# Kernel tuning notes

Hardware: AMD Instinct MI355X
Metric: run time of the kernel (lower is better)

The kernel has to match this reference:

```python
import jax, jax.numpy as jnp
import numpy as np
import math

B, S, H, NH = 1, 2048, 1024, 16  # batch, seq, hidden, heads


def setup_inputs() -> dict:
    key = jax.random.key(0)
    ks = jax.random.split(key, 12)
    inp = {
        "query": jax.random.normal(ks[0], (B, S, H), dtype=jnp.float32),
        "key": jax.random.normal(ks[1], (B, S, H), dtype=jnp.float32),
        "value": jax.random.normal(ks[2], (B, S, H), dtype=jnp.float32),
        "attention_mask": jax.random.randint(ks[3], (1, 1, S, S), 0, 2, dtype=jnp.int32),
        # torch nn.Linear params: y = x @ W.T + b, W init ~ U(-1/sqrt(H), 1/sqrt(H))
        "Wq": jax.random.uniform(ks[4], (H, H), jnp.float32, -1, 1) / math.sqrt(H),
        "bq": jax.random.uniform(ks[5], (H,), jnp.float32, -1, 1) / math.sqrt(H),
        "Wk": jax.random.uniform(ks[6], (H, H), jnp.float32, -1, 1) / math.sqrt(H),
        "bk": jax.random.uniform(ks[7], (H,), jnp.float32, -1, 1) / math.sqrt(H),
        "Wv": jax.random.uniform(ks[8], (H, H), jnp.float32, -1, 1) / math.sqrt(H),
        "bv": jax.random.uniform(ks[9], (H,), jnp.float32, -1, 1) / math.sqrt(H),
        "Wo": jax.random.uniform(ks[10], (H, H), jnp.float32, -1, 1) / math.sqrt(H),
        "bo": jax.random.uniform(ks[11], (H,), jnp.float32, -1, 1) / math.sqrt(H),
        "head": NH,
        "hidden_size": H,
    }
    return inp


def reference(query, key, value, attention_mask, Wq, bq, Wk, bk, Wv, bv, Wo, bo, head, hidden_size):
    b, s, _ = query.shape
    d_k = hidden_size // head

    def proj(x, W, bias):
        # [b, s, hidden] -> [b, head, s, d_k]
        y = x @ W.T + bias
        return y.reshape(b, s, head, d_k).transpose(0, 2, 1, 3)

    q = proj(query, Wq, bq)
    k = proj(key, Wk, bk)
    v = proj(value, Wv, bv)

    # naive full score matrix, as in the source (scale by sqrt(d_k) = last dim of q)
    scores = jnp.einsum("bhqd,bhkd->bhqk", q, k) / math.sqrt(d_k)
    # faithful quirk: masked positions are set to 0 (not -inf) before softmax
    scores = jnp.where(attention_mask == 0, jnp.zeros((), scores.dtype), scores)
    attn = jax.nn.softmax(scores, axis=-1)

    out = jnp.einsum("bhqk,bhkd->bhqd", attn, v)  # [b, head, s, d_k]
    out = out.transpose(0, 2, 1, 3).reshape(b, s, head * d_k)
    return out @ Wo.T + bo
```

## Files before the change

### kernel.cpp

```cpp
#include <hip/hip_runtime.h>
#include <hip/hip_bf16.h>


#define S_LEN 2048
#define HID   1024
#define NHEAD 16
#define DK    64

typedef unsigned short u16;
typedef __attribute__((ext_vector_type(8))) short bf16x8;
typedef __attribute__((ext_vector_type(4))) short bf16x4;
typedef __attribute__((ext_vector_type(4))) float f32x4;

__device__ __forceinline__ void load16_lds(const void* g, void* l) {
  __builtin_amdgcn_global_load_lds(
      (const __attribute__((address_space(1))) void*)g,
      (__attribute__((address_space(3))) void*)l, 16, 0, 0);
}

__device__ __forceinline__ short bfbits(float x) {
  __hip_bfloat16 h = __float2bfloat16(x);
  return *(short*)&h;
}
__device__ __forceinline__ bf16x8 cvt8(float4 a, float4 b) {
  bf16x8 r;
  r[0] = bfbits(a.x); r[1] = bfbits(a.y); r[2] = bfbits(a.z); r[3] = bfbits(a.w);
  r[4] = bfbits(b.x); r[5] = bfbits(b.y); r[6] = bfbits(b.z); r[7] = bfbits(b.w);
  return r;
}
__device__ __forceinline__ float bf2f(u16 u) {
  unsigned v = (unsigned)u << 16;
  return *(float*)&v;
}

__global__ __launch_bounds__(256) void cvtW_kernel(
    const float* __restrict__ wq, const float* __restrict__ wk,
    const float* __restrict__ wv, const float* __restrict__ wo,
    u16* __restrict__ Wbf) {
  const int y = blockIdx.y;
  const float* src = y == 0 ? wq : (y == 1 ? wk : (y == 2 ? wv : wo));
  size_t i = ((size_t)blockIdx.x * 256 + threadIdx.x) * 8;
  float4 a = *(const float4*)(src + i);
  float4 b = *(const float4*)(src + i + 4);
  *(bf16x8*)(Wbf + (size_t)y * (HID * HID) + i) = cvt8(a, b);
}

__global__ void pack_mask_kernel(const int* __restrict__ mask,
                                 unsigned int* __restrict__ bits) {
  int w = blockIdx.x * blockDim.x + threadIdx.x;
  const int4* p = (const int4*)(mask + (size_t)w * 32);
  unsigned word = 0;
#pragma unroll
  for (int i = 0; i < 8; ++i) {
    int4 v = p[i];
    word |= (unsigned)(v.x != 0) << (i * 4 + 0);
    word |= (unsigned)(v.y != 0) << (i * 4 + 1);
    word |= (unsigned)(v.z != 0) << (i * 4 + 2);
    word |= (unsigned)(v.w != 0) << (i * 4 + 3);
  }
  bits[w] = word;
}

template <int BM, bool ABF>
__global__ __launch_bounds__(512) void gemm_bt(
    const void* A0, const void* A1, const void* A2,
    const u16* __restrict__ Wbase,
    const float* b0, const float* b1, const float* b2,
    void* C0, void* C1, void* C2,
    int store_fp32, int transpose_z2, int qscale_z0) {
  constexpr int Mm = 2048, Nn = 1024, Kk = 1024, BK = 64;
  constexpr int NIT = Kk / BK;
  constexpr int MT = BM / 32;
  constexpr int MTILES = Mm / BM;
  constexpr int AG = BM / 16;
  constexpr int AU = BM / 64;

  const int z = blockIdx.z;
  const void* A    = z == 0 ? A0 : (z == 1 ? A1 : A2);
  const u16*  W    = Wbase + (size_t)z * (Nn * Kk);
  const float* bias = z == 0 ? b0 : (z == 1 ? b1 : b2);
  void*       C    = z == 0 ? C0 : (z == 1 ? C1 : C2);
  const int transpose = (z == 2) ? transpose_z2 : 0;
  const float oscale = (z == 0 && qscale_z0) ? 0.125f : 1.0f;

  const int tid = threadIdx.x, lane = tid & 63, wave = tid >> 6;
  const int q4 = lane >> 4, c16 = lane & 15;
  const int bLin = blockIdx.x + blockIdx.y * gridDim.x;
  const int mBase = (bLin % MTILES) * BM;
  const int nBase = (bLin / MTILES) * 128;
  const int wm = (wave >> 2) * (BM / 2), wn = (wave & 3) * 32;

  __shared__ __align__(16) u16 As[2][2][BM * 32];
  __shared__ __align__(16) u16 Bs[2][2][128 * 32];

  f32x4 acc[MT][2] = {};

  const int srow = lane >> 2;
  const int se8  = (lane & 3) * 8;

  const u16*   Ab = (const u16*)A;
  const float* Af = (const float*)A;

  auto issueW = [&](int it, int buf) {
#pragma unroll
    for (int j = 0; j < 2; ++j) {
      int u = wave * 2 + j;
      int h = u >> 3, grp = u & 7;
      load16_lds(W + (size_t)(nBase + grp * 16 + srow) * Kk + it * BK +
                     h * 32 + se8,
                 &Bs[buf][h][grp * 512]);
    }
  };
  auto issueA = [&](int it, int buf) {
#pragma unroll
    for (int j = 0; j < AU; ++j) {
      int u = wave * AU + j;
      int h = u / AG, grp = u % AG;
      load16_lds(Ab + (size_t)(mBase + grp * 16 + srow) * Kk + it * BK +
                     h * 32 + se8,
                 &As[buf][h][grp * 512]);
    }
  };
  float4 ar[AU][2];
  auto loadA = [&](int it) {
#pragma unroll
    for (int j = 0; j < AU; ++j) {
      int u = wave * AU + j;
      int h = u / AG, grp = u % AG;
      const float* s = Af + (size_t)(mBase + grp * 16 + srow) * Kk + it * BK +
                       h * 32 + se8;
      ar[j][0] = *(const float4*)s;
      ar[j][1] = *(const float4*)(s + 4);
    }
  };
  auto storeA = [&](int buf) {
#pragma unroll
    for (int j = 0; j < AU; ++j) {
      int u = wave * AU + j;
      int h = u / AG, grp = u % AG;
      *(bf16x8*)&As[buf][h][grp * 512 + srow * 32 + se8] =
          cvt8(ar[j][0], ar[j][1]);
    }
  };

  issueW(0, 0);
  if (ABF) issueA(0, 0);
  else { loadA(0); storeA(0); }
  __syncthreads();

  for (int it = 0; it < NIT; ++it) {
    const int buf = it & 1, nbuf = buf ^ 1;
    if (it + 1 < NIT) {
      issueW(it + 1, nbuf);
      if (ABF) issueA(it + 1, nbuf);
      else     loadA(it + 1);
    }
#pragma unroll
    for (int kk = 0; kk < 2; ++kk) {
      bf16x8 af[MT], bfr[2];
#pragma unroll
      for (int t = 0; t < MT; ++t)
        af[t] = *(const bf16x8*)&As[buf][kk][(wm + t * 16 + c16) * 32 + q4 * 8];
#pragma unroll
      for (int t = 0; t < 2; ++t)
        bfr[t] = *(const bf16x8*)&Bs[buf][kk][(wn + t * 16 + c16) * 32 + q4 * 8];
#pragma unroll
      for (int mt = 0; mt < MT; ++mt)
#pragma unroll
        for (int nt = 0; nt < 2; ++nt)
          acc[mt][nt] = __builtin_amdgcn_mfma_f32_16x16x32_bf16(
              af[mt], bfr[nt], acc[mt][nt], 0, 0, 0);
    }
    if (!ABF && it + 1 < NIT) storeA(nbuf);
    __syncthreads();
  }

#pragma unroll
  for (int nt = 0; nt < 2; ++nt) {
    int col = nBase + wn + nt * 16 + c16;
    float bv = bias[col];
#pragma unroll
    for (int mt = 0; mt < MT; ++mt) {
#pragma unroll
      for (int r = 0; r < 4; ++r) {
        int row = mBase + wm + mt * 16 + q4 * 4 + r;
        float v = (acc[mt][nt][r] + bv) * oscale;
        if (store_fp32)
          ((float*)C)[(size_t)row * Nn + col] = v;
        else if (transpose)
          ((__hip_bfloat16*)C)[(size_t)col * Mm + row] = __float2bfloat16(v);
        else
          ((__hip_bfloat16*)C)[(size_t)row * Nn + col] = __float2bfloat16(v);
      }
    }
  }
}

__global__ __launch_bounds__(512) void attn_kernel(
    const u16* __restrict__ Qb, const u16* __restrict__ Kb,
    const u16* __restrict__ Vt, const unsigned* __restrict__ mbits,
    u16* __restrict__ partO, float* __restrict__ partL) {
  constexpr int NITA = S_LEN / 2 / 64;
  const int qt = blockIdx.x, h = blockIdx.y, zz = blockIdx.z;
  const int tid = threadIdx.x, lane = tid & 63, wave = tid >> 6;
  const int q4 = lane >> 4, c16 = lane & 15;

  __shared__ __align__(16) u16 Ks[2][2][64 * 32];
  __shared__ __align__(16) u16 Vs[2][2][64 * 32];
  __shared__ __align__(16) u16 Ps[8][16 * 72];

  const int wq0 = qt * 128 + wave * 16;

  bf16x8 qf[2];
#pragma unroll
  for (int kk = 0; kk < 2; ++kk)
    qf[kk] = *(const bf16x8*)(Qb + (size_t)(wq0 + c16) * HID + h * DK +
                              kk * 32 + q4 * 8);

  f32x4 o[4] = {};
  float l_lane[4] = {};

  const int srow = lane >> 2;
  const int se8  = (lane & 3) * 8;
  const int kvbase = zz * (S_LEN / 2);

  auto issueKV = [&](int it, int buf) {
    const int kv0 = kvbase + it * 64;
#pragma unroll
    for (int j = 0; j < 2; ++j) {
      int i = wave * 2 + j;
      if (i < 8) {
        int half = i >> 2, grp = i & 3;
        load16_lds(Kb + (size_t)(kv0 + grp * 16 + srow) * HID + h * DK +
                       half * 32 + se8,
                   &Ks[buf][half][grp * 512]);
      } else {
        int ii = i - 8;
        int half = ii >> 2, grp = ii & 3;
        load16_lds(Vt + (size_t)(h * DK + grp * 16 + srow) * S_LEN + kv0 +
                       half * 32 + se8,
                   &Vs[buf][half][grp * 512]);
      }
    }
  };

  issueKV(0, 0);
  __syncthreads();

  for (int it = 0; it < NITA; ++it) {
    const int buf = it & 1, nbuf = buf ^ 1;
    const int kv0 = kvbase + it * 64;
    if (it + 1 < NITA) issueKV(it + 1, nbuf);

    f32x4 sv[4];
#pragma unroll
    for (int nt = 0; nt < 4; ++nt) {
      bf16x8 kf0 = *(const bf16x8*)&Ks[buf][0][(nt * 16 + c16) * 32 + q4 * 8];
      bf16x8 kf1 = *(const bf16x8*)&Ks[buf][1][(nt * 16 + c16) * 32 + q4 * 8];
      f32x4 a = {};
      a = __builtin_amdgcn_mfma_f32_16x16x32_bf16(qf[0], kf0, a, 0, 0, 0);
      a = __builtin_amdgcn_mfma_f32_16x16x32_bf16(qf[1], kf1, a, 0, 0, 0);
      sv[nt] = a;
    }

#pragma unroll
    for (int r = 0; r < 4; ++r) {
      int row = wq0 + q4 * 4 + r;
      const unsigned* mrow = mbits + (size_t)row * 64 + (kv0 >> 5);
      unsigned w0 = mrow[0], w1 = mrow[1];
#pragma unroll
      for (int nt = 0; nt < 4; ++nt) {
        unsigned word = (nt < 2) ? w0 : w1;
        int bit = ((nt & 1) * 16) + c16;
        float s = ((word >> bit) & 1u) ? sv[nt][r] : 0.0f;
        float p = __expf(s);
        sv[nt][r] = p;
        l_lane[r] += p;
      }
    }

    u16* pw = &Ps[wave][0];
#pragma unroll
    for (int r = 0; r < 4; ++r)
#pragma unroll
      for (int nt = 0; nt < 4; ++nt)
        ((__hip_bfloat16*)pw)[(q4 * 4 + r) * 72 + nt * 16 + c16] =
            __float2bfloat16(sv[nt][r]);
    asm volatile("s_waitcnt lgkmcnt(0)" ::: "memory");

#pragma unroll
    for (int kk = 0; kk < 2; ++kk) {
      bf16x8 pa = *(const bf16x8*)&pw[c16 * 72 + kk * 32 + q4 * 8];
#pragma unroll
      for (int nt = 0; nt < 4; ++nt) {
        bf16x8 vb = *(const bf16x8*)&Vs[buf][kk][(nt * 16 + c16) * 32 + q4 * 8];
        o[nt] = __builtin_amdgcn_mfma_f32_16x16x32_bf16(pa, vb, o[nt], 0, 0, 0);
      }
    }
    __syncthreads();
  }

#pragma unroll
  for (int r = 0; r < 4; ++r) {
    float s = l_lane[r];
#pragma unroll
    for (int d = 1; d < 16; d <<= 1) s += __shfl_xor(s, d);
    l_lane[r] = s;
  }

#pragma unroll
  for (int r = 0; r < 4; ++r) {
    int row = wq0 + q4 * 4 + r;
#pragma unroll
    for (int nt = 0; nt < 4; ++nt)
      ((__hip_bfloat16*)partO)[((size_t)zz * S_LEN + row) * HID + h * DK +
                               nt * 16 + c16] = __float2bfloat16(o[nt][r]);
    if (c16 == 0)
      partL[((size_t)zz * NHEAD + h) * S_LEN + row] = l_lane[r];
  }
}

__global__ __launch_bounds__(256) void combine_kernel(
    const u16* __restrict__ partO, const float* __restrict__ partL,
    u16* __restrict__ ctx) {
  size_t idx = ((size_t)blockIdx.x * 256 + threadIdx.x) * 4;
  int row = (int)(idx >> 10);
  int col = (int)(idx & 1023);
  int h = col >> 6;
  float l = partL[(size_t)h * S_LEN + row] +
            partL[((size_t)NHEAD + h) * S_LEN + row];
  float inv = 1.0f / l;
  bf16x4 a = *(const bf16x4*)(partO + idx);
  bf16x4 b = *(const bf16x4*)(partO + (size_t)S_LEN * HID + idx);
  bf16x4 r;
#pragma unroll
  for (int j = 0; j < 4; ++j) {
    float v = (bf2f((u16)a[j]) + bf2f((u16)b[j])) * inv;
    r[j] = bfbits(v);
  }
  *(bf16x4*)(ctx + idx) = r;
}

extern "C" void kernel_launch(void* const* d_in, const int* in_sizes, int n_in,
                              void* d_out, int out_size, void* d_ws, size_t ws_size,
                              hipStream_t stream) {
  const float* q    = (const float*)d_in[0];
  const float* k    = (const float*)d_in[1];
  const float* v    = (const float*)d_in[2];
  const int*   mask = (const int*)d_in[3];
  const float* Wq = (const float*)d_in[4];
  const float* bq = (const float*)d_in[5];
  const float* Wk = (const float*)d_in[6];
  const float* bk = (const float*)d_in[7];
  const float* Wv = (const float*)d_in[8];
  const float* bv = (const float*)d_in[9];
  const float* Wo = (const float*)d_in[10];
  const float* bo = (const float*)d_in[11];

  const size_t M2 = (size_t)S_LEN * HID;
  const size_t need = (4 + 2 + 2 + 2 + 2) * M2 * 2 +
                      (size_t)S_LEN * 64 * 4 + 2 * NHEAD * S_LEN * 4;
  if (ws_size < need) return;

  u16* Wbf   = (u16*)d_ws;
  u16* partO = Wbf + 4 * (size_t)HID * HID / 2 * 2;
  u16* Qb    = partO + 2 * M2;
  u16* Kb    = Qb + M2;
  u16* Vt    = Kb + M2;
  unsigned* mbits = (unsigned*)(Vt + M2);
  float* partL = (float*)(mbits + (size_t)S_LEN * 64);
  u16* ctx = Qb;

  hipLaunchKernelGGL(cvtW_kernel, dim3(512, 4), dim3(256), 0, stream,
                     Wq, Wk, Wv, Wo, Wbf);

  hipLaunchKernelGGL(pack_mask_kernel, dim3((S_LEN * (S_LEN / 32)) / 256),
                     dim3(256), 0, stream, mask, mbits);

  hipLaunchKernelGGL((gemm_bt<128, false>), dim3(8, 16, 3), dim3(512), 0,
                     stream, q, k, v, Wbf, bq, bk, bv,
                     (void*)Qb, (void*)Kb, (void*)Vt, 0, 1, 1);

  hipLaunchKernelGGL(attn_kernel, dim3(S_LEN / 128, NHEAD, 2), dim3(512), 0,
                     stream, Qb, Kb, Vt, mbits, partO, partL);

  hipLaunchKernelGGL(combine_kernel, dim3((S_LEN * HID / 4) / 256), dim3(256),
                     0, stream, partO, partL, ctx);

  hipLaunchKernelGGL((gemm_bt<64, true>), dim3(8, 32, 1), dim3(512), 0,
                     stream, ctx, ctx, ctx, Wbf + 3 * (size_t)HID * HID,
                     bo, bo, bo, d_out, d_out, d_out, 1, 0, 0);
}
```

Before: 213.5 us.

## Pre-convert QKV inputs to bf16 and retile projection GEMMs with smaller blocks

Adds a pre-pass that converts the fp32 query/key/value activations to bf16 together with the weights, so the QKV GEMM can stream both operands into LDS with direct global-to-LDS loads instead of register-staged fp32 conversion. The QKV and output GEMMs become dedicated kernels with 256-thread blocks and smaller M tiles (64 and 32 rows), giving more blocks for better CU occupancy. The cost is an extra full read and write pass over the activations and less operand reuse per block.

```diff
diff --git a/kernel.cpp b/kernel.cpp
--- a/kernel.cpp
+++ b/kernel.cpp
@@ -33,16 +33,31 @@
   return *(float*)&v;
 }
 
-__global__ __launch_bounds__(256) void cvtW_kernel(
-    const float* __restrict__ wq, const float* __restrict__ wk,
-    const float* __restrict__ wv, const float* __restrict__ wo,
+__global__ __launch_bounds__(256) void cvt_kernel(
+    const float* __restrict__ q, const float* __restrict__ k,
+    const float* __restrict__ v, const float* __restrict__ wq,
+    const float* __restrict__ wk, const float* __restrict__ wv,
+    const float* __restrict__ wo, u16* __restrict__ Xbf,
     u16* __restrict__ Wbf) {
   const int y = blockIdx.y;
-  const float* src = y == 0 ? wq : (y == 1 ? wk : (y == 2 ? wv : wo));
   size_t i = ((size_t)blockIdx.x * 256 + threadIdx.x) * 8;
+  const float* src;
+  u16* dst;
+  size_t n;
+  if (y < 3) {
+    src = y == 0 ? q : (y == 1 ? k : v);
+    dst = Xbf + (size_t)y * (S_LEN * HID);
+    n = (size_t)S_LEN * HID;
+  } else {
+    int w = y - 3;
+    src = w == 0 ? wq : (w == 1 ? wk : (w == 2 ? wv : wo));
+    dst = Wbf + (size_t)w * (HID * HID);
+    n = (size_t)HID * HID;
+  }
+  if (i >= n) return;
   float4 a = *(const float4*)(src + i);
   float4 b = *(const float4*)(src + i + 4);
-  *(bf16x8*)(Wbf + (size_t)y * (HID * HID) + i) = cvt8(a, b);
+  *(bf16x8*)(dst + i) = cvt8(a, b);
 }
 
 __global__ void pack_mask_kernel(const int* __restrict__ mask,
@@ -61,133 +76,86 @@
   bits[w] = word;
 }
 
-template <int BM, bool ABF>
-__global__ __launch_bounds__(512) void gemm_bt(
-    const void* A0, const void* A1, const void* A2,
-    const u16* __restrict__ Wbase,
-    const float* b0, const float* b1, const float* b2,
-    void* C0, void* C1, void* C2,
-    int store_fp32, int transpose_z2, int qscale_z0) {
-  constexpr int Mm = 2048, Nn = 1024, Kk = 1024, BK = 64;
-  constexpr int NIT = Kk / BK;
-  constexpr int MT = BM / 32;
-  constexpr int MTILES = Mm / BM;
-  constexpr int AG = BM / 16;
-  constexpr int AU = BM / 64;
-
+__global__ __launch_bounds__(256) void gemm_qkv(
+    const u16* __restrict__ Xbf, const u16* __restrict__ Wbf,
+    const float* __restrict__ bq, const float* __restrict__ bk,
+    const float* __restrict__ bv, u16* __restrict__ Qb,
+    u16* __restrict__ Kb, u16* __restrict__ Vt) {
+  constexpr int Mm = 2048, Nn = 1024, Kk = 1024, NIT = 16;
   const int z = blockIdx.z;
-  const void* A    = z == 0 ? A0 : (z == 1 ? A1 : A2);
-  const u16*  W    = Wbase + (size_t)z * (Nn * Kk);
-  const float* bias = z == 0 ? b0 : (z == 1 ? b1 : b2);
-  void*       C    = z == 0 ? C0 : (z == 1 ? C1 : C2);
-  const int transpose = (z == 2) ? transpose_z2 : 0;
-  const float oscale = (z == 0 && qscale_z0) ? 0.125f : 1.0f;
+  const u16* A = Xbf + (size_t)z * (S_LEN * HID);
+  const u16* W = Wbf + (size_t)z * (HID * HID);
+  const float* bias = z == 0 ? bq : (z == 1 ? bk : bv);
+  u16* C = z == 0 ? Qb : (z == 1 ? Kb : Vt);
+  const float oscale = (z == 0) ? 0.125f : 1.0f;
+  const int transpose = (z == 2);
 
   const int tid = threadIdx.x, lane = tid & 63, wave = tid >> 6;
   const int q4 = lane >> 4, c16 = lane & 15;
-  const int bLin = blockIdx.x + blockIdx.y * gridDim.x;
-  const int mBase = (bLin % MTILES) * BM;
-  const int nBase = (bLin / MTILES) * 128;
-  const int wm = (wave >> 2) * (BM / 2), wn = (wave & 3) * 32;
-
-  __shared__ __align__(16) u16 As[2][2][BM * 32];
+  const int bx = blockIdx.x;
+  const int mBase = (bx & 31) * 64;
+  const int nBase = (bx >> 5) * 128;
+  const int wn = wave * 32;
+
+  __shared__ __align__(16) u16 As[2][2][64 * 32];
   __shared__ __align__(16) u16 Bs[2][2][128 * 32];
 
-  f32x4 acc[MT][2] = {};
-
-  const int srow = lane >> 2;
-  const int se8  = (lane & 3) * 8;
-
-  const u16*   Ab = (const u16*)A;
-  const float* Af = (const float*)A;
-
-  auto issueW = [&](int it, int buf) {
+  f32x4 acc[4][2] = {};
+  const int srow = lane >> 2, se8 = (lane & 3) * 8;
+
+  auto issue = [&](int it, int buf) {
 #pragma unroll
     for (int j = 0; j < 2; ++j) {
-      int u = wave * 2 + j;
-      int h = u >> 3, grp = u & 7;
-      load16_lds(W + (size_t)(nBase + grp * 16 + srow) * Kk + it * BK +
+      int u = wave * 2 + j, h = u >> 2, grp = u & 3;
+      load16_lds(A + (size_t)(mBase + grp * 16 + srow) * Kk + it * 64 +
+                     h * 32 + se8,
+                 &As[buf][h][grp * 512]);
+    }
+#pragma unroll
+    for (int j = 0; j < 4; ++j) {
+      int u = wave * 4 + j, h = u >> 3, grp = u & 7;
+      load16_lds(W + (size_t)(nBase + grp * 16 + srow) * Kk + it * 64 +
                      h * 32 + se8,
                  &Bs[buf][h][grp * 512]);
     }
   };
-  auto issueA = [&](int it, int buf) {
-#pragma unroll
-    for (int j = 0; j < AU; ++j) {
-      int u = wave * AU + j;
-      int h = u / AG, grp = u % AG;
-      load16_lds(Ab + (size_t)(mBase + grp * 16 + srow) * Kk + it * BK +
-                     h * 32 + se8,
-                 &As[buf][h][grp * 512]);
-    }
-  };
-  float4 ar[AU][2];
-  auto loadA = [&](int it) {
-#pragma unroll
-    for (int j = 0; j < AU; ++j) {
-      int u = wave * AU + j;
-      int h = u / AG, grp = u % AG;
-      const float* s = Af + (size_t)(mBase + grp * 16 + srow) * Kk + it * BK +
-                       h * 32 + se8;
-      ar[j][0] = *(const float4*)s;
-      ar[j][1] = *(const float4*)(s + 4);
-    }
-  };
-  auto storeA = [&](int buf) {
-#pragma unroll
-    for (int j = 0; j < AU; ++j) {
-      int u = wave * AU + j;
-      int h = u / AG, grp = u % AG;
-      *(bf16x8*)&As[buf][h][grp * 512 + srow * 32 + se8] =
-          cvt8(ar[j][0], ar[j][1]);
-    }
-  };
-
-  issueW(0, 0);
-  if (ABF) issueA(0, 0);
-  else { loadA(0); storeA(0); }
+
+  issue(0, 0);
   __syncthreads();
 
   for (int it = 0; it < NIT; ++it) {
     const int buf = it & 1, nbuf = buf ^ 1;
-    if (it + 1 < NIT) {
-      issueW(it + 1, nbuf);
-      if (ABF) issueA(it + 1, nbuf);
-      else     loadA(it + 1);
-    }
+    if (it + 1 < NIT) issue(it + 1, nbuf);
 #pragma unroll
     for (int kk = 0; kk < 2; ++kk) {
-      bf16x8 af[MT], bfr[2];
-#pragma unroll
-      for (int t = 0; t < MT; ++t)
-        af[t] = *(const bf16x8*)&As[buf][kk][(wm + t * 16 + c16) * 32 + q4 * 8];
+      bf16x8 af[4], bfr[2];
+#pragma unroll
+      for (int t = 0; t < 4; ++t)
+        af[t] = *(const bf16x8*)&As[buf][kk][(t * 16 + c16) * 32 + q4 * 8];
 #pragma unroll
       for (int t = 0; t < 2; ++t)
         bfr[t] = *(const bf16x8*)&Bs[buf][kk][(wn + t * 16 + c16) * 32 + q4 * 8];
 #pragma unroll
-      for (int mt = 0; mt < MT; ++mt)
+      for (int mt = 0; mt < 4; ++mt)
 #pragma unroll
         for (int nt = 0; nt < 2; ++nt)
           acc[mt][nt] = __builtin_amdgcn_mfma_f32_16x16x32_bf16(
               af[mt], bfr[nt], acc[mt][nt], 0, 0, 0);
     }
-    if (!ABF && it + 1 < NIT) storeA(nbuf);
     __syncthreads();
   }
 
 #pragma unroll
   for (int nt = 0; nt < 2; ++nt) {
     int col = nBase + wn + nt * 16 + c16;
-    float bv = bias[col];
-#pragma unroll
-    for (int mt = 0; mt < MT; ++mt) {
+    float bv2 = bias[col];
+#pragma unroll
+    for (int mt = 0; mt < 4; ++mt) {
 #pragma unroll
       for (int r = 0; r < 4; ++r) {
-        int row = mBase + wm + mt * 16 + q4 * 4 + r;
-        float v = (acc[mt][nt][r] + bv) * oscale;
-        if (store_fp32)
-          ((float*)C)[(size_t)row * Nn + col] = v;
-        else if (transpose)
+        int row = mBase + mt * 16 + q4 * 4 + r;
+        float v = (acc[mt][nt][r] + bv2) * oscale;
+        if (transpose)
           ((__hip_bfloat16*)C)[(size_t)col * Mm + row] = __float2bfloat16(v);
         else
           ((__hip_bfloat16*)C)[(size_t)row * Nn + col] = __float2bfloat16(v);
@@ -339,6 +307,78 @@
     r[j] = bfbits(v);
   }
   *(bf16x4*)(ctx + idx) = r;
+}
+
+__global__ __launch_bounds__(256) void gemm_out(
+    const u16* __restrict__ ctx, const u16* __restrict__ Wo,
+    const float* __restrict__ bo, float* __restrict__ out) {
+  constexpr int Nn = 1024, Kk = 1024, NIT = 16;
+  const int tid = threadIdx.x, lane = tid & 63, wave = tid >> 6;
+  const int q4 = lane >> 4, c16 = lane & 15;
+  const int bx = blockIdx.x;
+  const int mBase = (bx & 63) * 32;
+  const int nBase = (bx >> 6) * 128;
+  const int wn = wave * 32;
+
+  __shared__ __align__(16) u16 As[2][2][32 * 32];
+  __shared__ __align__(16) u16 Bs[2][2][128 * 32];
+
+  f32x4 acc[2][2] = {};
+  const int srow = lane >> 2, se8 = (lane & 3) * 8;
+
+  auto issue = [&](int it, int buf) {
+    {
+      int u = wave, h = u >> 1, grp = u & 1;
+      load16_lds(ctx + (size_t)(mBase + grp * 16 + srow) * Kk + it * 64 +
+                     h * 32 + se8,
+                 &As[buf][h][grp * 512]);
+    }
+#pragma unroll
+    for (int j = 0; j < 4; ++j) {
+      int u = wave * 4 + j, h = u >> 3, grp = u & 7;
+      load16_lds(Wo + (size_t)(nBase + grp * 16 + srow) * Kk + it * 64 +
+                     h * 32 + se8,
+                 &Bs[buf][h][grp * 512]);
+    }
+  };
+
+  issue(0, 0);
+  __syncthreads();
+
+  for (int it = 0; it < NIT; ++it) {
+    const int buf = it & 1, nbuf = buf ^ 1;
+    if (it + 1 < NIT) issue(it + 1, nbuf);
+#pragma unroll
+    for (int kk = 0; kk < 2; ++kk) {
+      bf16x8 af[2], bfr[2];
+#pragma unroll
+      for (int t = 0; t < 2; ++t)
+        af[t] = *(const bf16x8*)&As[buf][kk][(t * 16 + c16) * 32 + q4 * 8];
+#pragma unroll
+      for (int t = 0; t < 2; ++t)
+        bfr[t] = *(const bf16x8*)&Bs[buf][kk][(wn + t * 16 + c16) * 32 + q4 * 8];
+#pragma unroll
+      for (int mt = 0; mt < 2; ++mt)
+#pragma unroll
+        for (int nt = 0; nt < 2; ++nt)
+          acc[mt][nt] = __builtin_amdgcn_mfma_f32_16x16x32_bf16(
+              af[mt], bfr[nt], acc[mt][nt], 0, 0, 0);
+    }
+    __syncthreads();
+  }
+
+#pragma unroll
+  for (int nt = 0; nt < 2; ++nt) {
+    int col = nBase + wn + nt * 16 + c16;
+    float bv = bo[col];
+#pragma unroll
+    for (int mt = 0; mt < 2; ++mt)
+#pragma unroll
+      for (int r = 0; r < 4; ++r) {
+        int row = mBase + mt * 16 + q4 * 4 + r;
+        out[(size_t)row * Nn + col] = acc[mt][nt][r] + bv;
+      }
+  }
 }
 
 extern "C" void kernel_launch(void* const* d_in, const int* in_sizes, int n_in,
@@ -358,28 +398,29 @@
   const float* bo = (const float*)d_in[11];
 
   const size_t M2 = (size_t)S_LEN * HID;
-  const size_t need = (4 + 2 + 2 + 2 + 2) * M2 * 2 +
+  const size_t W1 = (size_t)HID * HID;
+  const size_t need = (4 * W1 + 3 * M2 + 3 * M2) * 2 +
                       (size_t)S_LEN * 64 * 4 + 2 * NHEAD * S_LEN * 4;
   if (ws_size < need) return;
 
-  u16* Wbf   = (u16*)d_ws;
-  u16* partO = Wbf + 4 * (size_t)HID * HID / 2 * 2;
-  u16* Qb    = partO + 2 * M2;
-  u16* Kb    = Qb + M2;
-  u16* Vt    = Kb + M2;
+  u16* Wbf = (u16*)d_ws;
+  u16* Xbf = Wbf + 4 * W1;
+  u16* partO = Xbf;
+  u16* Qb = Xbf + 3 * M2;
+  u16* Kb = Qb + M2;
+  u16* Vt = Kb + M2;
   unsigned* mbits = (unsigned*)(Vt + M2);
   float* partL = (float*)(mbits + (size_t)S_LEN * 64);
   u16* ctx = Qb;
 
-  hipLaunchKernelGGL(cvtW_kernel, dim3(512, 4), dim3(256), 0, stream,
-                     Wq, Wk, Wv, Wo, Wbf);
+  hipLaunchKernelGGL(cvt_kernel, dim3(1024, 7), dim3(256), 0, stream,
+                     q, k, v, Wq, Wk, Wv, Wo, Xbf, Wbf);
 
   hipLaunchKernelGGL(pack_mask_kernel, dim3((S_LEN * (S_LEN / 32)) / 256),
                      dim3(256), 0, stream, mask, mbits);
 
-  hipLaunchKernelGGL((gemm_bt<128, false>), dim3(8, 16, 3), dim3(512), 0,
-                     stream, q, k, v, Wbf, bq, bk, bv,
-                     (void*)Qb, (void*)Kb, (void*)Vt, 0, 1, 1);
+  hipLaunchKernelGGL(gemm_qkv, dim3(256, 1, 3), dim3(256), 0, stream,
+                     Xbf, Wbf, bq, bk, bv, Qb, Kb, Vt);
 
   hipLaunchKernelGGL(attn_kernel, dim3(S_LEN / 128, NHEAD, 2), dim3(512), 0,
                      stream, Qb, Kb, Vt, mbits, partO, partL);
@@ -387,7 +428,6 @@
   hipLaunchKernelGGL(combine_kernel, dim3((S_LEN * HID / 4) / 256), dim3(256),
                      0, stream, partO, partL, ctx);
 
-  hipLaunchKernelGGL((gemm_bt<64, true>), dim3(8, 32, 1), dim3(512), 0,
-                     stream, ctx, ctx, ctx, Wbf + 3 * (size_t)HID * HID,
-                     bo, bo, bo, d_out, d_out, d_out, 1, 0, 0);
-}
+  hipLaunchKernelGGL(gemm_out, dim3(512), dim3(256), 0, stream,
+                     ctx, Wbf + 3 * W1, bo, (float*)d_out);
+}
```

After: 202.5 us. 1.05x faster.
